# Kernel optimization log

Hardware: AMD Instinct MI355X
Metric: run time of the kernel (lower is better)

## Reference

```python
import jax, jax.numpy as jnp
import numpy as np
import math

# static config (see shape_source)
NUM_GRAPHS = 8      # b
L_NODES = 1024      # nodes per graph (uniform -> to_dense_batch is a reshape)
D_INNER = 128
HEADDIM = 16
N_HEADS = D_INNER // HEADDIM  # 8
D_STATE = 64
NUM_DT = 4          # 3 node-dt components + dt_self
AVG_DEG = 16
DIAMETER = 50       # default_graph_diameter
TOL = 0.1
DT_MIN, DT_MAX, DT_FLOOR = 1e-3, 1e-1, 1e-4


def dag_inverse(A):
    """DAGInverse.forward: (I - A)^{-1} via repeated-squaring doubling.
    A: [b, h, l, l]. j = 2^ceil(log2(diameter)); out = prod (I + A^{2^k})."""
    j = 2 ** math.ceil(math.log2(DIAMETER))  # 64
    I = jnp.eye(A.shape[-1], dtype=A.dtype)
    last = A
    out = I + A
    for _ in range(2, int(math.log2(j)) + 1):  # 5 iterations
        last = last @ last
        out = out @ (I + last)
    return out


def setup_inputs() -> dict:
    key = jax.random.key(0)
    k = jax.random.split(key, 8)
    N = NUM_GRAPHS * L_NODES
    x = jax.random.normal(k[0], (N, D_INNER), jnp.float32)
    B_mat = jax.random.normal(k[1], (N, D_STATE), jnp.float32)
    C_mat = jax.random.normal(k[2], (N, D_STATE), jnp.float32)
    dt = jax.random.normal(k[3], (N, NUM_DT * N_HEADS), jnp.float32)
    # dt_bias init as in GraphSSD.__init__
    u = jax.random.uniform(k[4], (N_HEADS,), jnp.float32)
    dt0 = jnp.exp(u * (math.log(DT_MAX) - math.log(DT_MIN)) + math.log(DT_MIN))
    dt0 = jnp.clip(dt0, DT_FLOOR, None)
    dt_bias = dt0 + jnp.log(-jnp.expm1(-dt0))
    D = jnp.ones((N_HEADS,), jnp.float32)
    # edges: per-graph random endpoints, offset to global node ids
    E_per = L_NODES * AVG_DEG
    src_l = jax.random.randint(k[5], (NUM_GRAPHS, E_per), 0, L_NODES)
    dst_l = jax.random.randint(k[6], (NUM_GRAPHS, E_per), 0, L_NODES)
    off = (jnp.arange(NUM_GRAPHS) * L_NODES)[:, None]
    edge_index = jnp.stack([(src_l + off).reshape(-1), (dst_l + off).reshape(-1)], 0).astype(jnp.int32)
    return {"x": x, "B_mat": B_mat, "C_mat": C_mat, "dt": dt,
            "dt_bias": dt_bias, "D": D, "edge_index": edge_index}


def reference(x, B_mat, C_mat, dt, dt_bias, D, edge_index):
    Bn, Lg, H, hd, ds = NUM_GRAPHS, L_NODES, N_HEADS, HEADDIM, D_STATE
    N = Bn * Lg
    # dense batching (uniform graph sizes -> pure reshape, mask all True)
    x_d = x.reshape(Bn, Lg, H, hd).transpose(0, 2, 1, 3)        # b n l h ('(n h)' split)
    B_d = B_mat.reshape(Bn, Lg, ds)                             # broadcast over heads
    C_d = C_mat.reshape(Bn, Lg, ds)
    # dt: 'l (n c) -> c n l'
    dt_c = dt.reshape(N, H, NUM_DT).transpose(2, 1, 0)          # c n l
    dt_node, dt_self = dt_c[:NUM_DT - 1], dt_c[NUM_DT - 1]      # (3,n,N), (n,N)
    dt_self_d = dt_self.T.reshape(Bn, Lg, H).transpose(0, 2, 1)  # b n l
    # multiply_dt_w_A: A = -exp(A_log)= -1 (with_A=False)
    dt_A_node = -jax.nn.softplus(dt_node + dt_bias[None, :, None])  # (3, n, N)
    # edge dt: (dt_s[src] + dt_t[dst]) / 2, then exp
    src, dst = edge_index[0], edge_index[1]
    attr = jnp.exp((dt_A_node[0][:, src] + dt_A_node[1][:, dst]) * 0.5).T  # (E, n)
    # to_dense_adj scatter: [b, l1, l2, h] then -> b h l1 l2
    b_idx, sl, dl = src // Lg, src % Lg, dst % Lg
    A_mat = jnp.zeros((Bn, Lg, Lg, H), x.dtype).at[b_idx, sl, dl].add(attr)
    A_mat = A_mat.transpose(0, 3, 1, 2)                          # b n l1 l2
    # 'leq' normalization with dummy self term
    dt_dummy = jnp.exp(dt_A_node[2]).T.reshape(Bn, Lg, H).transpose(0, 2, 1)  # b n l
    normalizer = A_mat.sum(-1) + dt_dummy                        # b n l1
    A_norm = A_mat / (normalizer[..., None] + TOL)
    # L = (I - A^T)^{-1} via DAGInverse doubling
    Lmat = dag_inverse(jnp.swapaxes(A_norm, -1, -2).astype(jnp.float32))  # b n l t
    L_norm = Lmat * dt_self_d[:, :, None, :]                     # scale along t
    # y = einsum(C, L, B, x); C/B broadcast in heads -> G shared across heads
    G = jnp.einsum('bld,btd->blt', C_d, B_d)[:, None]            # b 1 l t
    y = jnp.einsum('bnlt,bnth->bnlh', L_norm * G, x_d)
    y = y + x_d * D[None, :, None, None]
    # 'b n l h -> b l (h n)'
    y = y.transpose(0, 2, 3, 1).reshape(Bn, Lg, H * hd)
    return y.reshape(N, H * hd)
```

## Files before the change

kernel.cpp:

```cpp
#include <hip/hip_runtime.h>
#include <hip/hip_bf16.h>

#define H_ 8
#define NTOT 8192
#define LG 1024
#define BN 8
#define HD 16
#define DSTATE 64
#define EPG 16384
#define MSZ (1024*1024)

typedef __hip_bfloat16 bf16;
typedef unsigned short ushort_t;
typedef _Float16 f16;
typedef __attribute__((ext_vector_type(8))) _Float16 half8;
typedef __attribute__((ext_vector_type(4))) _Float16 half4;
typedef __attribute__((ext_vector_type(4))) float f4v;

__device__ __forceinline__ float b2f(bf16 v){ return __bfloat162float(v); }
__device__ __forceinline__ float sp_(float z){
  return fmaxf(z, 0.f) + log1pf(expf(-fabsf(z)));
}
__device__ __forceinline__ float ldv(const void* p, size_t i, int f32){
  float v;
  if (f32) v = ((const float*)p)[i];
  else     v = b2f(((const bf16*)p)[i]);
  return v;
}
__device__ __forceinline__ unsigned ldsaddr(const void* p){
  return (unsigned)(uintptr_t)(__attribute__((address_space(3))) const char*)p;
}

#define BARC() do { asm volatile("" ::: "memory"); __builtin_amdgcn_s_barrier(); asm volatile("" ::: "memory"); } while(0)
#define SB0() __builtin_amdgcn_sched_barrier(0)
#define DSR(dst, base, off) asm volatile("ds_read_b128 %0, %1 offset:" #off : "=v"(dst) : "v"(base))
#define GLD(p, d) __builtin_amdgcn_global_load_lds((const __attribute__((address_space(1))) unsigned int*)(p), \
    (__attribute__((address_space(3))) unsigned int*)(d), 16, 0, 0)

__global__ void k_sniff(const void* __restrict__ dt, int* __restrict__ flag){
  const ushort_t* p = (const ushort_t*)dt;
  int tid = threadIdx.x;
  int bad = 0;
  for (int i = tid; i < 512; i += 256){
    int e = (p[i] >> 7) & 0xFF;
    if (e >= 140) bad = 1;
  }
  unsigned long long m = __ballot(bad != 0);
  __shared__ int anybad[4];
  if ((tid & 63) == 0) anybad[tid >> 6] = (m != 0ull) ? 1 : 0;
  __syncthreads();
  if (tid == 0) *flag = (anybad[0] | anybad[1] | anybad[2] | anybad[3]);
}

__global__ void k_nodecoef(const void* __restrict__ dt, const void* __restrict__ dtb,
                           const int* __restrict__ flag,
                           float* __restrict__ a0, float* __restrict__ a1,
                           float* __restrict__ dum, float* __restrict__ sdt){
  int idx = blockIdx.x*256 + threadIdx.x;
  if (idx >= H_*NTOT) return;
  int f32 = *flag;
  int h = idx / NTOT, n = idx - h*NTOT;
  float bias = ldv(dtb, h, f32);
  size_t base = (size_t)n*(4*H_) + h*4;
  float d0, d1, d2, d3;
  if (f32){
    const float* row = (const float*)dt + base;
    d0 = row[0]; d1 = row[1]; d2 = row[2]; d3 = row[3];
  } else {
    const bf16* row = (const bf16*)dt + base;
    d0 = b2f(row[0]); d1 = b2f(row[1]); d2 = b2f(row[2]); d3 = b2f(row[3]);
  }
  a0[(size_t)n*H_ + h] = -sp_(d0 + bias);
  a1[(size_t)n*H_ + h] = -sp_(d1 + bias);
  dum[idx] = expf(-sp_(d2 + bias));
  sdt[idx] = d3;
}

__global__ __launch_bounds__(256) void k_zero(char* base, size_t regB, float* __restrict__ nrm){
  int bh = blockIdx.y;
  if (blockIdx.x < 1024){
    float* Mf = (float*)(base + (size_t)bh*regB) + MSZ;
    int i = blockIdx.x*1024 + threadIdx.x*4;
    *(float4*)(Mf + i) = make_float4(0.f,0.f,0.f,0.f);
  } else {
    int j = threadIdx.x*4;
    *(float4*)(nrm + (size_t)bh*LG + j) = make_float4(0.f,0.f,0.f,0.f);
  }
}

__global__ void k_scatter(const int* __restrict__ ei, const float* __restrict__ a0,
                          const float* __restrict__ a1, char* base, size_t regB,
                          float* __restrict__ nrm,
                          int b0, int h0, int lgHB, int GBp, int nthreads, int Etot){
  int t = blockIdx.x*256 + threadIdx.x;
  if (t >= nthreads) return;
  int HB = 1 << lgHB;
  int hl = t & (HB-1);
  int el = t >> lgHB;
  int e = b0*EPG + el;
  int src = ei[e], dst = ei[Etot + e];
  int g = src >> 10;
  if ((unsigned)(g - b0) >= (unsigned)GBp) return;
  int sl = src & 1023, dl = dst & 1023;
  int h = h0 + hl;
  float attr = expf(0.5f*(a0[(size_t)src*H_ + h] + a1[(size_t)dst*H_ + h]));
  int bhl = (g - b0)*HB + hl;
  float* Mf = (float*)(base + (size_t)bhl*regB) + MSZ;
  atomicAdd(&Mf[(size_t)dl*LG + sl], attr);
  atomicAdd(&nrm[bhl*LG + sl], attr);
}

__global__ __launch_bounds__(256) void k_norm2(char* base, size_t regB,
                            const float* __restrict__ nrm, const float* __restrict__ dum,
                            int b0, int h0, int HB){
  __shared__ ushort_t tb[32][33];
  int bh = blockIdx.z;
  int g = b0 + bh / HB, h = h0 + bh % HB;
  const float* Mf = (const float*)(base + (size_t)bh*regB) + MSZ;
  f16* L0  = (f16*)(base + (size_t)bh*regB);
  f16* L0T = L0 + MSZ;
  f16* O0  = L0 + (size_t)4*MSZ;
  int x0 = blockIdx.x*32, y0 = blockIdx.y*32;
  int tx = threadIdx.x & 31, ty = threadIdx.x >> 5;
  int sl = x0 + tx;
  float denom = nrm[(size_t)bh*LG + sl] + dum[(size_t)h*NTOT + g*LG + sl] + 0.1f;
  float rden = 1.f / denom;
  #pragma unroll
  for (int i = 0; i < 32; i += 8){
    int dl = y0 + ty + i;
    float v = Mf[(size_t)dl*LG + sl] * rden;
    f16 hv = (f16)v;
    L0[(size_t)dl*LG + sl] = hv;
    O0[(size_t)dl*LG + sl] = (f16)(v + (dl == sl ? 1.f : 0.f));
    union { f16 h; ushort_t u; } cv; cv.h = hv;
    tb[tx][ty + i] = cv.u;
  }
  __syncthreads();
  #pragma unroll
  for (int i = 0; i < 32; i += 8){
    union { f16 h; ushort_t u; } cv; cv.u = tb[ty + i][tx];
    L0T[(size_t)(x0 + ty + i)*LG + y0 + tx] = cv.h;
  }
}

__global__ __launch_bounds__(256) void k_G(const void* __restrict__ Bm, const void* __restrict__ Cm,
                                           const int* __restrict__ flag,
                                           f16* __restrict__ G, int b0){
  int gl = blockIdx.z;
  int g = b0 + gl;
  int l0 = blockIdx.y*16, t0 = blockIdx.x*16;
  __shared__ float Cs[16][DSTATE+1];
  __shared__ float Bs[16][DSTATE+1];
  int tid = threadIdx.x;
  int f32 = *flag;
  if (f32){
    const float* Cf = (const float*)Cm;
    const float* Bf = (const float*)Bm;
    for (int i = tid; i < 16*DSTATE; i += 256){
      int r = i >> 6, d = i & 63;
      Cs[r][d] = Cf[(size_t)(g*LG + l0 + r)*DSTATE + d];
      Bs[r][d] = Bf[(size_t)(g*LG + t0 + r)*DSTATE + d];
    }
  } else {
    const bf16* Cb = (const bf16*)Cm;
    const bf16* Bb = (const bf16*)Bm;
    for (int i = tid; i < 16*DSTATE; i += 256){
      int r = i >> 6, d = i & 63;
      Cs[r][d] = b2f(Cb[(size_t)(g*LG + l0 + r)*DSTATE + d]);
      Bs[r][d] = b2f(Bb[(size_t)(g*LG + t0 + r)*DSTATE + d]);
    }
  }
  __syncthreads();
  int r = tid >> 4, c = tid & 15;
  float acc = 0.f;
  #pragma unroll
  for (int d = 0; d < DSTATE; ++d) acc = fmaf(Cs[r][d], Bs[c][d], acc);
  G[(size_t)gl*MSZ + (size_t)(l0+r)*LG + t0 + c] = (f16)acc;
}

#define RD_S0(s) do{ \
  DSR(af##s##0,aAlo,0);     DSR(af##s##1,aAlo,1024);  DSR(af##s##2,aAlo,2048);  DSR(af##s##3,aAlo,3072); \
  DSR(bf##s##0,aBlo,0);     DSR(bf##s##1,aBlo,1024);  DSR(bf##s##2,aBlo,2048);  DSR(bf##s##3,aBlo,3072); }while(0)
#define RD_S1(s) do{ \
  DSR(af##s##0,aAlo,24576); DSR(af##s##1,aAlo,25600); DSR(af##s##2,aAlo,26624); DSR(af##s##3,aAlo,27648); \
  DSR(bf##s##0,aBlo,24576); DSR(bf##s##1,aBlo,25600); DSR(bf##s##2,aBlo,26624); DSR(bf##s##3,aBlo,27648); }while(0)
#define RD_S2(s) do{ \
  DSR(af##s##0,aAhi,0);     DSR(af##s##1,aAhi,1024);  DSR(af##s##2,aAhi,2048);  DSR(af##s##3,aAhi,3072); \
  DSR(bf##s##0,aBhi,0);     DSR(bf##s##1,aBhi,1024);  DSR(bf##s##2,aBhi,2048);  DSR(bf##s##3,aBhi,3072); }while(0)
#define RD_S3(s) do{ \
  DSR(af##s##0,aAhi,24576); DSR(af##s##1,aAhi,25600); DSR(af##s##2,aAhi,26624); DSR(af##s##3,aAhi,27648); \
  DSR(bf##s##0,aBhi,24576); DSR(bf##s##1,aBhi,25600); DSR(bf##s##2,aBhi,26624); DSR(bf##s##3,aBhi,27648); }while(0)
#define MF1(s, m, n) acc[m][n] = __builtin_amdgcn_mfma_f32_16x16x32_f16(af##s##m, bf##s##n, acc[m][n], 0, 0, 0)
#define MFMA16(s) do{ \
  MF1(s,0,0); MF1(s,0,1); MF1(s,0,2); MF1(s,0,3); \
  MF1(s,1,0); MF1(s,1,1); MF1(s,1,2); MF1(s,1,3); \
  MF1(s,2,0); MF1(s,2,1); MF1(s,2,2); MF1(s,2,3); \
  MF1(s,3,0); MF1(s,3,1); MF1(s,3,2); MF1(s,3,3); }while(0)
#define ISS(SL, GOFF) do{ \
  GLD(pA  + (GOFF), dA  + (SL)); \
  GLD(pB0 + (GOFF), dB0 + (SL)); \
  GLD(pB1 + (GOFF), dB1 + (SL)); }while(0)
#define LGKM0() asm volatile("s_waitcnt lgkmcnt(0)" ::: "memory")
#define VM3()   asm volatile("s_waitcnt vmcnt(3)" ::: "memory")
#define VM0()   asm volatile("s_waitcnt vmcnt(0)" ::: "memory")

__global__ __launch_bounds__(512, 2) void k_gemm_fused(char* base, size_t regB,
    int nS, int iAs, int iBTs, int iCs, int iCTs,
    int nU, int iAu, int iBTu, int iCu){
  extern __shared__ char lds[];
  int T = nS + nU;
  int s = blockIdx.x + 8*blockIdx.z;
  if (s >= T) return;
  int isS = (s < nS) ? 1 : 0;
  int bh  = isS ? s : (s - nS);
  int iA  = isS ? iAs : iAu;
  int iBT = isS ? iBTs : iBTu;
  int iC  = isS ? iCs : iCu;
  int iCT = isS ? iCTs : -1;
  int addA = 1 - isS;
  char* reg = base + (size_t)bh*regB;
  const f16* Ab = (const f16*)reg + (size_t)iA*MSZ;
  const f16* Bb = (const f16*)reg + (size_t)iBT*MSZ;
  f16* Cb = (f16*)reg + (size_t)iC*MSZ;
  int y = blockIdx.y;
  int i0 = (y >> 2)*128, j0 = (y & 3)*256;
  int tid = threadIdx.x;
  int lane = tid & 63, wv = tid >> 6;
  int wm = wv >> 2, wn = wv & 3;
  int m16 = lane & 15, q = lane >> 4;
  unsigned swz = (unsigned)((q ^ ((m16 >> 1) & 3)) << 4);
  unsigned lbase = ldsaddr(lds);
  unsigned aAlo = lbase + (unsigned)((wm*64 + m16)*64) + swz;
  unsigned aBlo = lbase + 8192u + (unsigned)((wn*64 + m16)*64) + swz;
  unsigned aAhi = aAlo + 49152u;
  unsigned aBhi = aBlo + 49152u;
  int rs = tid >> 2;
  int cs = (tid & 3) ^ ((rs >> 1) & 3);
  const char* pA  = (const char*)(Ab + (size_t)(i0 + rs)*LG + cs*8);
  const char* pB0 = (const char*)(Bb + (size_t)(j0 + rs)*LG + cs*8);
  const char* pB1 = (const char*)(Bb + (size_t)(j0 + 128 + rs)*LG + cs*8);
  char* dA  = lds + (size_t)tid*16;
  char* dB0 = lds + 8192 + (size_t)tid*16;
  char* dB1 = lds + 16384 + (size_t)tid*16;

  f4v acc[4][4] = {};
  half8 af00, af01, af02, af03, bf00, bf01, bf02, bf03;
  half8 af10, af11, af12, af13, bf10, bf11, bf12, bf13;

  ISS(0, 0); ISS(24576, 64); ISS(49152, 128);
  asm volatile("s_waitcnt vmcnt(6)" ::: "memory");
  BARC();
  RD_S0(0);
  asm volatile("s_waitcnt lgkmcnt(0) vmcnt(3)" ::: "memory");
  BARC();

  for (int kt = 0; kt < 28; kt += 4){
    RD_S1(1); ISS(73728, 192); SB0();
    __builtin_amdgcn_s_setprio(1); MFMA16(0); __builtin_amdgcn_s_setprio(0); SB0();
    LGKM0(); VM3(); BARC();
    RD_S2(0); ISS(0, 256); SB0();
    __builtin_amdgcn_s_setprio(1); MFMA16(1); __builtin_amdgcn_s_setprio(0); SB0();
    LGKM0(); VM3(); BARC();
    RD_S3(1); ISS(24576, 320); SB0();
    __builtin_amdgcn_s_setprio(1); MFMA16(0); __builtin_amdgcn_s_setprio(0); SB0();
    LGKM0(); VM3(); BARC();
    RD_S0(0); ISS(49152, 384); SB0();
    __builtin_amdgcn_s_setprio(1); MFMA16(1); __builtin_amdgcn_s_setprio(0); SB0();
    LGKM0(); VM3(); BARC();
    pA += 256; pB0 += 256; pB1 += 256;
  }
  RD_S1(1); ISS(73728, 192); SB0();
  __builtin_amdgcn_s_setprio(1); MFMA16(0); __builtin_amdgcn_s_setprio(0); SB0();
  LGKM0(); VM3(); BARC();
  RD_S2(0); SB0();
  __builtin_amdgcn_s_setprio(1); MFMA16(1); __builtin_amdgcn_s_setprio(0); SB0();
  LGKM0(); VM0(); BARC();
  RD_S3(1); SB0();
  __builtin_amdgcn_s_setprio(1); MFMA16(0); __builtin_amdgcn_s_setprio(0); SB0();
  LGKM0(); BARC();
  __builtin_amdgcn_s_setprio(1); MFMA16(1); __builtin_amdgcn_s_setprio(0);

  f16* CT = (f16*)reg + (size_t)((iCT < 0) ? iC : iCT)*MSZ;
  #pragma unroll
  for (int mt = 0; mt < 4; ++mt){
    #pragma unroll
    for (int nt = 0; nt < 4; ++nt){
      int gr0 = i0 + wm*64 + mt*16 + q*4;
      int gc  = j0 + wn*64 + nt*16 + m16;
      half4 tv;
      #pragma unroll
      for (int r = 0; r < 4; ++r){
        float v = acc[mt][nt][r];
        if (addA) v += (float)Ab[(size_t)(gr0 + r)*LG + gc];
        f16 hv = (f16)v;
        tv[r] = hv;
        Cb[(size_t)(gr0 + r)*LG + gc] = hv;
      }
      if (iCT >= 0)
        *(half4*)&CT[(size_t)gc*LG + gr0] = tv;
    }
  }
}

__global__ __launch_bounds__(256) void k_final2(char* base, size_t regB, int iO,
    const f16* __restrict__ Gh, const float* __restrict__ sdt,
    const void* __restrict__ x, const void* __restrict__ Dv,
    const int* __restrict__ flag, void* __restrict__ out,
    int b0, int h0, int HB){
  __shared__ float coef[16][257];
  int bh = blockIdx.y;
  int gl = bh / HB, g = b0 + gl, h = h0 + bh % HB;
  int L0r = blockIdx.x*16;
  int tid = threadIdx.x;
  int lr = tid >> 4, ts = tid & 15;
  int f32 = *flag;
  const f16* Orow = (const f16*)(base + (size_t)bh*regB) + (size_t)iO*MSZ + (size_t)(L0r+lr)*LG;
  const f16* Grow = Gh + (size_t)gl*MSZ + (size_t)(L0r+lr)*LG;
  const float* srow = sdt + (size_t)h*NTOT + g*LG;
  float acc = 0.f;
  for (int tc = 0; tc < LG; tc += 256){
    int tb = tc + ts*16;
    __syncthreads();
    half8 o0 = *(const half8*)&Orow[tb];
    half8 o1 = *(const half8*)&Orow[tb + 8];
    half8 g0 = *(const half8*)&Grow[tb];
    half8 g1 = *(const half8*)&Grow[tb + 8];
    #pragma unroll
    for (int j = 0; j < 8; ++j){
      coef[lr][ts*16 + j]     = (float)o0[j] * (float)g0[j] * srow[tb + j];
      coef[lr][ts*16 + 8 + j] = (float)o1[j] * (float)g1[j] * srow[tb + 8 + j];
    }
    __syncthreads();
    if (f32){
      const float* xf = (const float*)x + (size_t)(g*LG + tc)*128 + h*HD + ts;
      for (int t = 0; t < 256; ++t)
        acc = fmaf(coef[lr][t], xf[(size_t)t*128], acc);
    } else {
      const bf16* xb = (const bf16*)x + (size_t)(g*LG + tc)*128 + h*HD + ts;
      for (int t = 0; t < 256; ++t)
        acc = fmaf(coef[lr][t], b2f(xb[(size_t)t*128]), acc);
    }
  }
  int l = L0r + lr, d = ts;
  float xs = ldv(x, (size_t)(g*LG + l)*128 + h*HD + d, f32);
  float dv = ldv(Dv, h, f32);
  float v = acc + xs*dv;
  size_t off = (size_t)(g*LG + l)*128 + d*H_ + h;
  if (f32) ((float*)out)[off] = v;
  else     ((bf16*)out)[off] = __float2bfloat16(v);
}

extern "C" void kernel_launch(void* const* d_in, const int* in_sizes, int n_in,
                              void* d_out, int out_size, void* d_ws, size_t ws_size,
                              hipStream_t stream){
  const void* x   = d_in[0];
  const void* Bm  = d_in[1];
  const void* Cm  = d_in[2];
  const void* dt  = d_in[3];
  const void* dtb = d_in[4];
  const void* Dv  = d_in[5];
  const int*  ei  = (const int*)d_in[6];
  int Etot = in_sizes[6] / 2;

  static int attrDone = 0;
  if (!attrDone){
    hipFuncSetAttribute(reinterpret_cast<const void*>(k_gemm_fused),
                        hipFuncAttributeMaxDynamicSharedMemorySize, 131072);
    attrDone = 1;
  }

  const size_t REG = (size_t)6*MSZ*2;
  int GB = 1, HB = 1;
  const int cfgs[7][2] = {{8,8},{4,8},{2,8},{1,8},{1,4},{1,2},{1,1}};
  for (int i = 0; i < 7; ++i){
    int gb = cfgs[i][0], hb = cfgs[i][1];
    size_t need = 4ull*(4ull*H_*NTOT + 64)
                + 4ull*(size_t)gb*hb*LG
                + 2ull*(size_t)gb*MSZ
                + (size_t)gb*hb*REG;
    if (need <= ws_size){ GB = gb; HB = hb; break; }
  }
  int lgHB = (HB==8)?3:((HB==4)?2:((HB==2)?1:0));
  int nbh = GB*HB;

  float* a0  = (float*)d_ws;
  float* a1  = a0 + H_*NTOT;
  float* dum = a1 + H_*NTOT;
  float* sdt = dum + H_*NTOT;
  int*  flag = (int*)(sdt + H_*NTOT);
  float* nrm = (float*)flag + 64;
  f16* G     = (f16*)(nrm + (size_t)nbh*LG);
  char* chainBase = (char*)(G + (size_t)GB*MSZ);

  k_sniff<<<1, 256, 0, stream>>>(dt, flag);
  k_nodecoef<<<(H_*NTOT + 255)/256, 256, 0, stream>>>(dt, dtb, flag, a0, a1, dum, sdt);

  for (int b0 = 0; b0 < BN; b0 += GB){
    for (int h0 = 0; h0 < H_; h0 += HB){
      k_zero<<<dim3(1025, nbh), 256, 0, stream>>>(chainBase, REG, nrm);
      int nthr = GB*EPG*HB;
      k_scatter<<<(nthr + 255)/256, 256, 0, stream>>>(ei, a0, a1, chainBase, REG, nrm,
                                                      b0, h0, lgHB, GB, nthr, Etot);
      k_norm2<<<dim3(32, 32, nbh), 256, 0, stream>>>(chainBase, REG, nrm, dum, b0, h0, HB);
      if (h0 == 0){
        dim3 gg(64, 64, GB);
        k_G<<<gg, 256, 0, stream>>>(Bm, Cm, flag, G, b0);
      }
      int lA = 0, lAT = 1, lC = 2, lCT = 3, oA = 4, oC = 5;
      {
        int T = nbh;
        dim3 gg(8, 32, (T + 7)/8);
        k_gemm_fused<<<gg, 512, 98304, stream>>>(chainBase, REG, nbh, lA, lAT, lC, lCT,
                                                 0, 0, 0, 0);
      }
      for (int k = 0; k < 4; ++k){
        int T = 2*nbh;
        dim3 gg(8, 32, (T + 7)/8);
        k_gemm_fused<<<gg, 512, 98304, stream>>>(chainBase, REG,
                                                 nbh, lC, lCT, lA, lAT,
                                                 nbh, oA, lCT, oC);
        int tp;
        tp = lA; lA = lC; lC = tp;
        tp = lAT; lAT = lCT; lCT = tp;
        tp = oA; oA = oC; oC = tp;
      }
      {
        int T = nbh;
        dim3 gg(8, 32, (T + 7)/8);
        k_gemm_fused<<<gg, 512, 98304, stream>>>(chainBase, REG, 0, 0, 0, 0, 0,
                                                 nbh, oA, lCT, oC);
        int tp = oA; oA = oC; oC = tp;
      }
      dim3 fg(64, nbh);
      k_final2<<<fg, 256, 0, stream>>>(chainBase, REG, oA, G, sdt, x, Dv, flag, d_out, b0, h0, HB);
    }
  }
}
```

Before: 2.625 ms.

## Load GEMM A operand directly to registers, triple-buffer B in smaller LDS

The fused GEMM kernel now loads A-tile fragments straight from global memory into registers with global_load_dwordx4, rather than staging them through LDS. Only B is staged, through a 3-slot LDS ring, which cuts dynamic LDS from 96KB to 48KB. Launch bounds rise to 4 blocks per SM to raise occupancy. The cost is uncoalesced, per-wave redundant global loads of A, and a simpler single-register-set pipeline with a barrier every k-step.

After: 3.842 ms. +46.4%, slower.

```diff
diff --git a/kernel.cpp b/kernel.cpp
--- a/kernel.cpp
+++ b/kernel.cpp
@@ -34,6 +34,7 @@
 #define BARC() do { asm volatile("" ::: "memory"); __builtin_amdgcn_s_barrier(); asm volatile("" ::: "memory"); } while(0)
 #define SB0() __builtin_amdgcn_sched_barrier(0)
 #define DSR(dst, base, off) asm volatile("ds_read_b128 %0, %1 offset:" #off : "=v"(dst) : "v"(base))
+#define GLA(dst, ptr, off) asm volatile("global_load_dwordx4 %0, %1, off offset:" #off : "=v"(dst) : "v"(ptr))
 #define GLD(p, d) __builtin_amdgcn_global_load_lds((const __attribute__((address_space(1))) unsigned int*)(p), \
     (__attribute__((address_space(3))) unsigned int*)(d), 16, 0, 0)
 
@@ -178,33 +179,17 @@
   G[(size_t)gl*MSZ + (size_t)(l0+r)*LG + t0 + c] = (f16)acc;
 }
 
-#define RD_S0(s) do{ \
-  DSR(af##s##0,aAlo,0);     DSR(af##s##1,aAlo,1024);  DSR(af##s##2,aAlo,2048);  DSR(af##s##3,aAlo,3072); \
-  DSR(bf##s##0,aBlo,0);     DSR(bf##s##1,aBlo,1024);  DSR(bf##s##2,aBlo,2048);  DSR(bf##s##3,aBlo,3072); }while(0)
-#define RD_S1(s) do{ \
-  DSR(af##s##0,aAlo,24576); DSR(af##s##1,aAlo,25600); DSR(af##s##2,aAlo,26624); DSR(af##s##3,aAlo,27648); \
-  DSR(bf##s##0,aBlo,24576); DSR(bf##s##1,aBlo,25600); DSR(bf##s##2,aBlo,26624); DSR(bf##s##3,aBlo,27648); }while(0)
-#define RD_S2(s) do{ \
-  DSR(af##s##0,aAhi,0);     DSR(af##s##1,aAhi,1024);  DSR(af##s##2,aAhi,2048);  DSR(af##s##3,aAhi,3072); \
-  DSR(bf##s##0,aBhi,0);     DSR(bf##s##1,aBhi,1024);  DSR(bf##s##2,aBhi,2048);  DSR(bf##s##3,aBhi,3072); }while(0)
-#define RD_S3(s) do{ \
-  DSR(af##s##0,aAhi,24576); DSR(af##s##1,aAhi,25600); DSR(af##s##2,aAhi,26624); DSR(af##s##3,aAhi,27648); \
-  DSR(bf##s##0,aBhi,24576); DSR(bf##s##1,aBhi,25600); DSR(bf##s##2,aBhi,26624); DSR(bf##s##3,aBhi,27648); }while(0)
-#define MF1(s, m, n) acc[m][n] = __builtin_amdgcn_mfma_f32_16x16x32_f16(af##s##m, bf##s##n, acc[m][n], 0, 0, 0)
-#define MFMA16(s) do{ \
-  MF1(s,0,0); MF1(s,0,1); MF1(s,0,2); MF1(s,0,3); \
-  MF1(s,1,0); MF1(s,1,1); MF1(s,1,2); MF1(s,1,3); \
-  MF1(s,2,0); MF1(s,2,1); MF1(s,2,2); MF1(s,2,3); \
-  MF1(s,3,0); MF1(s,3,1); MF1(s,3,2); MF1(s,3,3); }while(0)
-#define ISS(SL, GOFF) do{ \
-  GLD(pA  + (GOFF), dA  + (SL)); \
-  GLD(pB0 + (GOFF), dB0 + (SL)); \
-  GLD(pB1 + (GOFF), dB1 + (SL)); }while(0)
-#define LGKM0() asm volatile("s_waitcnt lgkmcnt(0)" ::: "memory")
-#define VM3()   asm volatile("s_waitcnt vmcnt(3)" ::: "memory")
-#define VM0()   asm volatile("s_waitcnt vmcnt(0)" ::: "memory")
-
-__global__ __launch_bounds__(512, 2) void k_gemm_fused(char* base, size_t regB,
+#define RD_B0 do{ DSR(bf0,aB,0);     DSR(bf1,aB,1024);  DSR(bf2,aB,2048);  DSR(bf3,aB,3072);  }while(0)
+#define RD_B1 do{ DSR(bf0,aB,16384); DSR(bf1,aB,17408); DSR(bf2,aB,18432); DSR(bf3,aB,19456); }while(0)
+#define RD_B2 do{ DSR(bf0,aB,32768); DSR(bf1,aB,33792); DSR(bf2,aB,34816); DSR(bf3,aB,35840); }while(0)
+#define MF1(m, n) acc[m][n] = __builtin_amdgcn_mfma_f32_16x16x32_f16(af##m, bf##n, acc[m][n], 0, 0, 0)
+#define MFMA16() do{ \
+  MF1(0,0); MF1(0,1); MF1(0,2); MF1(0,3); \
+  MF1(1,0); MF1(1,1); MF1(1,2); MF1(1,3); \
+  MF1(2,0); MF1(2,1); MF1(2,2); MF1(2,3); \
+  MF1(3,0); MF1(3,1); MF1(3,2); MF1(3,3); }while(0)
+
+__global__ __launch_bounds__(512, 4) void k_gemm_fused(char* base, size_t regB,
     int nS, int iAs, int iBTs, int iCs, int iCTs,
     int nU, int iAu, int iBTu, int iCu){
   extern __shared__ char lds[];
@@ -230,55 +215,52 @@
   int m16 = lane & 15, q = lane >> 4;
   unsigned swz = (unsigned)((q ^ ((m16 >> 1) & 3)) << 4);
   unsigned lbase = ldsaddr(lds);
-  unsigned aAlo = lbase + (unsigned)((wm*64 + m16)*64) + swz;
-  unsigned aBlo = lbase + 8192u + (unsigned)((wn*64 + m16)*64) + swz;
-  unsigned aAhi = aAlo + 49152u;
-  unsigned aBhi = aBlo + 49152u;
+  unsigned aB = lbase + (unsigned)((wn*64 + m16)*64) + swz;
+  const char* pA0 = (const char*)Ab + (size_t)(i0 + wm*64 +  0 + m16)*2048 + q*16;
+  const char* pA1 = (const char*)Ab + (size_t)(i0 + wm*64 + 16 + m16)*2048 + q*16;
+  const char* pA2 = (const char*)Ab + (size_t)(i0 + wm*64 + 32 + m16)*2048 + q*16;
+  const char* pA3 = (const char*)Ab + (size_t)(i0 + wm*64 + 48 + m16)*2048 + q*16;
   int rs = tid >> 2;
   int cs = (tid & 3) ^ ((rs >> 1) & 3);
-  const char* pA  = (const char*)(Ab + (size_t)(i0 + rs)*LG + cs*8);
   const char* pB0 = (const char*)(Bb + (size_t)(j0 + rs)*LG + cs*8);
   const char* pB1 = (const char*)(Bb + (size_t)(j0 + 128 + rs)*LG + cs*8);
-  char* dA  = lds + (size_t)tid*16;
-  char* dB0 = lds + 8192 + (size_t)tid*16;
-  char* dB1 = lds + 16384 + (size_t)tid*16;
+  char* dB0 = lds + (size_t)tid*16;
+  char* dB1 = lds + 8192 + (size_t)tid*16;
 
   f4v acc[4][4] = {};
-  half8 af00, af01, af02, af03, bf00, bf01, bf02, bf03;
-  half8 af10, af11, af12, af13, bf10, bf11, bf12, bf13;
-
-  ISS(0, 0); ISS(24576, 64); ISS(49152, 128);
-  asm volatile("s_waitcnt vmcnt(6)" ::: "memory");
+  half8 af0, af1, af2, af3, bf0, bf1, bf2, bf3;
+
+  GLD(pB0, dB0);        GLD(pB1, dB1);
+  GLD(pB0 + 64, dB0 + 16384); GLD(pB1 + 64, dB1 + 16384);
+  asm volatile("s_waitcnt vmcnt(2)" ::: "memory");
+
+  #define BODY(RDM, SWLIT, AOFF, PBOFF) do{ \
+    BARC(); \
+    GLA(af0, pA0, AOFF); GLA(af1, pA1, AOFF); GLA(af2, pA2, AOFF); GLA(af3, pA3, AOFF); \
+    GLD(pB0 + (PBOFF), dB0 + (SWLIT)); GLD(pB1 + (PBOFF), dB1 + (SWLIT)); \
+    RDM; \
+    asm volatile("s_waitcnt vmcnt(2) lgkmcnt(0)" ::: "memory"); SB0(); \
+    __builtin_amdgcn_s_setprio(1); MFMA16(); __builtin_amdgcn_s_setprio(0); SB0(); \
+  }while(0)
+
+  for (int t = 0; t < 10; ++t){
+    BODY(RD_B0, 32768, 0,   128);
+    BODY(RD_B1, 0,     64,  192);
+    BODY(RD_B2, 16384, 128, 256);
+    pA0 += 192; pA1 += 192; pA2 += 192; pA3 += 192;
+    pB0 += 192; pB1 += 192;
+  }
+  #undef BODY
   BARC();
-  RD_S0(0);
-  asm volatile("s_waitcnt lgkmcnt(0) vmcnt(3)" ::: "memory");
+  GLA(af0, pA0, 0); GLA(af1, pA1, 0); GLA(af2, pA2, 0); GLA(af3, pA3, 0);
+  RD_B0;
+  asm volatile("s_waitcnt vmcnt(0) lgkmcnt(0)" ::: "memory"); SB0();
+  __builtin_amdgcn_s_setprio(1); MFMA16(); __builtin_amdgcn_s_setprio(0); SB0();
   BARC();
-
-  for (int kt = 0; kt < 28; kt += 4){
-    RD_S1(1); ISS(73728, 192); SB0();
-    __builtin_amdgcn_s_setprio(1); MFMA16(0); __builtin_amdgcn_s_setprio(0); SB0();
-    LGKM0(); VM3(); BARC();
-    RD_S2(0); ISS(0, 256); SB0();
-    __builtin_amdgcn_s_setprio(1); MFMA16(1); __builtin_amdgcn_s_setprio(0); SB0();
-    LGKM0(); VM3(); BARC();
-    RD_S3(1); ISS(24576, 320); SB0();
-    __builtin_amdgcn_s_setprio(1); MFMA16(0); __builtin_amdgcn_s_setprio(0); SB0();
-    LGKM0(); VM3(); BARC();
-    RD_S0(0); ISS(49152, 384); SB0();
-    __builtin_amdgcn_s_setprio(1); MFMA16(1); __builtin_amdgcn_s_setprio(0); SB0();
-    LGKM0(); VM3(); BARC();
-    pA += 256; pB0 += 256; pB1 += 256;
-  }
-  RD_S1(1); ISS(73728, 192); SB0();
-  __builtin_amdgcn_s_setprio(1); MFMA16(0); __builtin_amdgcn_s_setprio(0); SB0();
-  LGKM0(); VM3(); BARC();
-  RD_S2(0); SB0();
-  __builtin_amdgcn_s_setprio(1); MFMA16(1); __builtin_amdgcn_s_setprio(0); SB0();
-  LGKM0(); VM0(); BARC();
-  RD_S3(1); SB0();
-  __builtin_amdgcn_s_setprio(1); MFMA16(0); __builtin_amdgcn_s_setprio(0); SB0();
-  LGKM0(); BARC();
-  __builtin_amdgcn_s_setprio(1); MFMA16(1); __builtin_amdgcn_s_setprio(0);
+  GLA(af0, pA0, 64); GLA(af1, pA1, 64); GLA(af2, pA2, 64); GLA(af3, pA3, 64);
+  RD_B1;
+  asm volatile("s_waitcnt vmcnt(0) lgkmcnt(0)" ::: "memory"); SB0();
+  __builtin_amdgcn_s_setprio(1); MFMA16(); __builtin_amdgcn_s_setprio(0); SB0();
 
   f16* CT = (f16*)reg + (size_t)((iCT < 0) ? iC : iCT)*MSZ;
   #pragma unroll
@@ -365,7 +347,7 @@
   static int attrDone = 0;
   if (!attrDone){
     hipFuncSetAttribute(reinterpret_cast<const void*>(k_gemm_fused),
-                        hipFuncAttributeMaxDynamicSharedMemorySize, 131072);
+                        hipFuncAttributeMaxDynamicSharedMemorySize, 65536);
     attrDone = 1;
   }
 
@@ -410,13 +392,13 @@
       {
         int T = nbh;
         dim3 gg(8, 32, (T + 7)/8);
-        k_gemm_fused<<<gg, 512, 98304, stream>>>(chainBase, REG, nbh, lA, lAT, lC, lCT,
+        k_gemm_fused<<<gg, 512, 49152, stream>>>(chainBase, REG, nbh, lA, lAT, lC, lCT,
                                                  0, 0, 0, 0);
       }
       for (int k = 0; k < 4; ++k){
         int T = 2*nbh;
         dim3 gg(8, 32, (T + 7)/8);
-        k_gemm_fused<<<gg, 512, 98304, stream>>>(chainBase, REG,
+        k_gemm_fused<<<gg, 512, 49152, stream>>>(chainBase, REG,
                                                  nbh, lC, lCT, lA, lAT,
                                                  nbh, oA, lCT, oC);
         int tp;
@@ -427,7 +409,7 @@
       {
         int T = nbh;
         dim3 gg(8, 32, (T + 7)/8);
-        k_gemm_fused<<<gg, 512, 98304, stream>>>(chainBase, REG, 0, 0, 0, 0, 0,
+        k_gemm_fused<<<gg, 512, 49152, stream>>>(chainBase, REG, 0, 0, 0, 0, 0,
                                                  nbh, oA, lCT, oC);
         int tp = oA; oA = oC; oC = tp;
       }
```
